# Optimization experiments

Hardware: AMD Instinct MI355X
Metric: run time of the kernel (lower is better)

## Reference

```python
import jax, jax.numpy as jnp
import numpy as np

N = 50000       # nodes
E = 1600000     # edges
H = 64          # hidden_channels
G = 16          # graphs in batch
DOUT = 2        # dim_out
NODE_IN = 1
EDGE_IN = 3


def setup_inputs() -> dict:
    key = jax.random.key(0)
    ks = jax.random.split(key, 24)
    p = lambda k, shape: (jax.random.normal(k, shape, jnp.float32) * 0.05)
    inp = {
        "x": jax.random.normal(ks[0], (N, NODE_IN), jnp.float32),
        "edge_index": jax.random.randint(ks[1], (2, E), 0, N, dtype=jnp.int64),
        "edge_attr": jax.random.normal(ks[2], (E, EDGE_IN), jnp.float32),
        "batch": jnp.sort(jax.random.randint(ks[3], (N,), 0, G, dtype=jnp.int64)),
        # EdgeModel MLP: Linear(2*node_in+edge_in, H), ReLU, Linear(H, H)
        "ew1": p(ks[4], (2 * NODE_IN + EDGE_IN, H)), "eb1": p(ks[5], (H,)),
        "ew2": p(ks[6], (H, H)), "eb2": p(ks[7], (H,)),
        # NodeModel MLP: Linear(node_in+edge_out, H), ReLU, Linear(H, H)
        "nw1": p(ks[8], (NODE_IN + H, H)), "nb1": p(ks[9], (H,)),
        "nw2": p(ks[10], (H, H)), "nb2": p(ks[11], (H,)),
        "ow1": p(ks[12], (H, H)), "ob1": p(ks[13], (H,)),
        "ow2": p(ks[14], (H, H)), "ob2": p(ks[15], (H,)),
        "ow3": p(ks[16], (H, H)), "ob3": p(ks[17], (H,)),
        "ow4": p(ks[18], (H, DOUT)), "ob4": p(ks[19], (DOUT,)),
    }
    return inp


def reference(x, edge_index, edge_attr, batch,
              ew1, eb1, ew2, eb2,
              nw1, nb1, nw2, nb2,
              ow1, ob1, ow2, ob2, ow3, ob3, ow4, ob4):
    row, col = edge_index[0], edge_index[1]
    # EdgeModel: gather endpoints, concat, 2-layer MLP (no residual)
    e_in = jnp.concatenate([x[row], x[col], edge_attr], axis=1)      # [E, 2+3]
    e = jax.nn.relu(e_in @ ew1 + eb1) @ ew2 + eb2                    # [E, H]
    # NodeModel: scatter_add edge messages into destination nodes
    agg = jax.ops.segment_sum(e, col, num_segments=x.shape[0])      # [N, H]
    h_in = jnp.concatenate([x, agg], axis=1)                         # [N, 1+H]
    h = jax.nn.relu(h_in @ nw1 + nb1) @ nw2 + nb2                    # [N, H]
    # global_add_pool over graphs
    pooled = jax.ops.segment_sum(h, batch, num_segments=G)          # [G, H]
    o = jax.nn.relu(pooled @ ow1 + ob1)
    o = jax.nn.relu(o @ ow2 + ob2)
    o = jax.nn.relu(o @ ow3 + ob3)
    return o @ ow4 + ob4                                             # [G, DOUT]
```

## Files before the change

kernel.cpp:

```cpp
#include <hip/hip_runtime.h>
#include <hip/hip_bf16.h>

#define HID 64
#define NGRAPH 16
#define BN 32
#define GB 8
#define MAXNB 2048
#define NCB 256
#define NCT 1024
#define SORT_T 1024
#define SORT_CHUNK 12800

typedef __attribute__((ext_vector_type(8))) short short8;
typedef __attribute__((ext_vector_type(4))) float f32x4;

enum : int {
  OFF_V      = 1040,
  OFF_M      = 1104,
  OFF_EW1    = 5200,
  OFF_EB1    = 5520,
  OFF_NW1    = 5584,
  OFF_NB1    = 9744,
  OFF_NW2    = 9808,
  OFF_NB2    = 13904,
  OFF_OW1    = 13968,
  OFF_OB1    = 18064,
  OFF_OW2    = 18128,
  OFF_OB2    = 22224,
  OFF_OW3    = 22288,
  OFF_OB3    = 26384,
  OFF_OW4    = 26448,
  OFF_OB4    = 26576,
  OFF_EW2    = 26580,
  OFF_EB2    = 30676,
  OFF_FLAGS  = 30740,
  OFF_W1T    = 30744,
  OFF_MT     = 31000,
  OFF_PREP   = 33048
};

struct WPtrs { const void* p[16]; };

__device__ __forceinline__ float cv(float v) { return v; }
__device__ __forceinline__ float cv(__hip_bfloat16 v) { return __bfloat162float(v); }
__device__ __forceinline__ float b2f(unsigned short u) {
  union { unsigned u32; float f; } c;
  c.u32 = ((unsigned)u) << 16;
  return c.f;
}
__device__ __forceinline__ unsigned short f2bu(float v) {
  union { __hip_bfloat16 b; unsigned short u; } c;
  c.b = __float2bfloat16(v);
  return c.u;
}
__device__ __forceinline__ unsigned short fr(float v) {
  unsigned u = __float_as_uint(v);
  u += 0x7FFFu + ((u >> 16) & 1u);
  return (unsigned short)(u >> 16);
}
__device__ __forceinline__ unsigned rndpack(float a, float b) {
  unsigned ua = __float_as_uint(fmaxf(a, 0.0f));
  unsigned ub = __float_as_uint(fmaxf(b, 0.0f));
  ua += 0x7FFFu + ((ua >> 16) & 1u);
  ub += 0x7FFFu + ((ub >> 16) & 1u);
  return __builtin_amdgcn_perm(ub, ua, 0x07060302u);
}

__global__ __launch_bounds__(1024) void prep_kernel(
    const void* xv, const void* eiv, WPtrs wp, float* ws)
{
  __shared__ int red[2];
  __shared__ int s_ft;
  __shared__ float ew2s[4096];
  __shared__ float nw1s[4096];
  const int t = threadIdx.x;
  const int lane = t & 63;

  if (t == 0) { red[0] = 0; red[1] = 0; }
  __syncthreads();
  {
    int big = 0;
    if (t < 512) {
      const unsigned el = (((const unsigned*)xv)[t] >> 7) & 0xFFu;
      big = (el >= 140u) ? 1 : 0;
    }
    #pragma unroll
    for (int o = 32; o > 0; o >>= 1) big += __shfl_xor(big, o);
    if (lane == 0 && big) atomicAdd(&red[0], big);
  }
  {
    int orv = ((const int*)eiv)[1 + 2 * t];
    #pragma unroll
    for (int o = 32; o > 0; o >>= 1) orv |= __shfl_xor(orv, o);
    if (lane == 0 && orv) atomicOr(&red[1], orv);
  }
  __syncthreads();
  if (t == 0) {
    const int ft = (red[0] < 8) ? 1 : 0;
    const int it = (red[1] == 0) ? 1 : 0;
    ((int*)(ws + OFF_FLAGS))[0] = ft;
    ((int*)(ws + OFF_FLAGS))[1] = it;
    s_ft = ft;
  }
  __syncthreads();
  const int ft = s_ft;

  const int sz[16]  = {320,64,4096,64,4160,64,4096,64,4096,64,4096,64,4096,64,128,2};
  const int dst[16] = {OFF_EW1,OFF_EB1,OFF_EW2,OFF_EB2,OFF_NW1,OFF_NB1,OFF_NW2,OFF_NB2,
                       OFF_OW1,OFF_OB1,OFF_OW2,OFF_OB2,OFF_OW3,OFF_OB3,OFF_OW4,OFF_OB4};
  for (int a = 0; a < 16; ++a) {
    const void* src = wp.p[a];
    float* d = ws + dst[a];
    const int n = sz[a];
    const int n4 = n >> 2;
    for (int i = t; i < n4; i += 1024) {
      float4 f;
      if (ft) {
        const ushort4 u4 = ((const ushort4*)src)[i];
        f.x = b2f(u4.x); f.y = b2f(u4.y); f.z = b2f(u4.z); f.w = b2f(u4.w);
      } else {
        f = ((const float4*)src)[i];
      }
      ((float4*)d)[i] = f;
      const int g = i << 2;
      if (a == 2) {
        ew2s[g] = f.x; ew2s[g + 1] = f.y; ew2s[g + 2] = f.z; ew2s[g + 3] = f.w;
      } else if (a == 4 && g >= 64) {
        nw1s[g - 64] = f.x; nw1s[g - 63] = f.y; nw1s[g - 62] = f.z; nw1s[g - 61] = f.w;
      }
    }
    for (int i = (n4 << 2) + t; i < n; i += 1024)
      d[i] = ft ? b2f(((const unsigned short*)src)[i]) : ((const float*)src)[i];
  }
  __syncthreads();

  float mv[4];
  #pragma unroll
  for (int p = 0; p < 4; ++p) {
    const int idx = t + p * 1024;
    const int i = idx >> 6, j = idx & 63;
    float s = 0.0f;
    #pragma unroll 8
    for (int k = 0; k < 64; ++k)
      s = fmaf(ew2s[i * 64 + k], nw1s[k * 64 + j], s);
    mv[p] = s;
  }
  if (t < 64) {
    float s = 0.0f;
    #pragma unroll 8
    for (int k = 0; k < 64; ++k)
      s = fmaf(ws[OFF_EB2 + k], nw1s[k * 64 + t], s);
    ws[OFF_V + t] = s;
  }
  __syncthreads();
  #pragma unroll
  for (int p = 0; p < 4; ++p) ew2s[t + p * 1024] = mv[p];
  __syncthreads();

  if (t < 64) {
    unsigned short* w1t = (unsigned short*)(ws + OFF_W1T);
    #pragma unroll
    for (int k = 0; k < 8; ++k) {
      float v = 0.0f;
      if (k < 5) v = ws[OFF_EW1 + k * 64 + t];
      else if (k == 5) v = ws[OFF_EB1 + t];
      w1t[t * 8 + k] = f2bu(v);
    }
  }
  unsigned short* mt = (unsigned short*)(ws + OFF_MT);
  #pragma unroll
  for (int p = 0; p < 4; ++p) {
    const int idx = t + p * 1024;
    const int n = idx >> 6, k = idx & 63;
    mt[idx] = f2bu(ew2s[k * 64 + n]);
  }
}

template<typename IT>
__device__ __forceinline__ void count_impl(
    const IT* __restrict__ ei, const IT* __restrict__ bt,
    int* __restrict__ gcnt, int* __restrict__ endG, int* lh,
    const int E, const int N, const int NBG)
{
  const int t = threadIdx.x;
  const int b = blockIdx.x;
  for (int i = t; i < NBG; i += NCT) lh[i] = 0;
  {
    const int i = b * NCT + t;
    if (i < N) {
      const int g1 = (int)bt[i];
      if (i == 0) for (int g = 0; g < g1; ++g) endG[g] = 0;
      if (i == N - 1) {
        for (int g = g1; g < NGRAPH; ++g) endG[g] = N;
      } else {
        const int g2 = (int)bt[i + 1];
        for (int g = g1; g < g2; ++g) endG[g] = i + 1;
      }
    }
  }
  __syncthreads();
  const int per = (E + NCB - 1) / NCB;
  const int a = b * per;
  const int bnd = (a + per < E) ? (a + per) : E;
  for (int e = a + t; e < bnd; e += NCT) {
    const int c = (int)ei[(size_t)E + e];
    atomicAdd(&lh[c >> 8], 1);
  }
  __syncthreads();
  for (int i = t; i < NBG; i += NCT) gcnt[(size_t)i * NCB + b] = lh[i];
}

__global__ __launch_bounds__(NCT) void count_kernel(
    const void* eiv, const void* batv, const float* ws,
    int* gcnt, int* endG, const int E, const int N, const int NBG)
{
  __shared__ int lh[MAXNB];
  const int it = ((const int*)(ws + OFF_FLAGS))[1];
  if (it) count_impl<long long>((const long long*)eiv, (const long long*)batv, gcnt, endG, lh, E, N, NBG);
  else    count_impl<int>((const int*)eiv, (const int*)batv, gcnt, endG, lh, E, N, NBG);
}

__global__ __launch_bounds__(256) void scan_tot_kernel(
    const int* __restrict__ gcnt, int* __restrict__ gstart, const int NBG)
{
  const int lane = threadIdx.x & 63;
  const int bkt = blockIdx.x * 4 + (threadIdx.x >> 6);
  if (bkt >= NBG) return;
  const int4 v = *(const int4*)(gcnt + (size_t)bkt * NCB + lane * 4);
  int s = v.x + v.y + v.z + v.w;
  #pragma unroll
  for (int off = 32; off > 0; off >>= 1) s += __shfl_xor(s, off);
  if (lane == 0) gstart[bkt] = s;
}

__global__ __launch_bounds__(256) void scan_pref_kernel(
    int* __restrict__ gstart, const int NBG)
{
  __shared__ int ps[256];
  const int t = threadIdx.x;
  const int seg = (NBG + 255) / 256;
  int s = 0;
  for (int i = 0; i < seg; ++i) {
    const int idx = t * seg + i;
    if (idx < NBG) s += gstart[idx];
  }
  ps[t] = s;
  __syncthreads();
  for (int off = 1; off < 256; off <<= 1) {
    const int v = (t >= off) ? ps[t - off] : 0;
    __syncthreads();
    ps[t] += v;
    __syncthreads();
  }
  int carry = ps[t] - s;
  for (int i = 0; i < seg; ++i) {
    const int idx = t * seg + i;
    if (idx < NBG) {
      const int c = gstart[idx];
      gstart[idx] = carry;
      carry += c;
    }
  }
  if (t == 255) gstart[NBG] = ps[255];
}

__global__ __launch_bounds__(256) void scan_row_kernel(
    int* __restrict__ gcnt, const int* __restrict__ gstart, const int NBG)
{
  const int lane = threadIdx.x & 63;
  const int bkt = blockIdx.x * 4 + (threadIdx.x >> 6);
  if (bkt >= NBG) return;
  int* row = gcnt + (size_t)bkt * NCB;
  const int4 v = *(const int4*)(row + lane * 4);
  const int ls = v.x + v.y + v.z + v.w;
  int s = ls;
  #pragma unroll
  for (int off = 1; off < 64; off <<= 1) {
    const int u = __shfl_up(s, off);
    if (lane >= off) s += u;
  }
  int e = s - ls + gstart[bkt];
  int4 o;
  o.x = e; e += v.x;
  o.y = e; e += v.y;
  o.z = e; e += v.z;
  o.w = e;
  *(int4*)(row + lane * 4) = o;
}

template<typename FT, typename IT>
__device__ __forceinline__ void scatter_impl(
    const FT* __restrict__ x, const IT* __restrict__ ei, const FT* __restrict__ ea,
    const int* __restrict__ gcnt, const int* __restrict__ gstart,
    ushort4* __restrict__ recB, unsigned char* __restrict__ cid, int* lb,
    const int E, const int gb0, const int gb1, const int cap)
{
  const int t = threadIdx.x;
  const int b = blockIdx.x;
  __shared__ int sbase;
  if (t == 0) sbase = gstart[gb0];
  __syncthreads();
  const int base = sbase;
  const int gcount = gb1 - gb0;
  for (int i = t; i < gcount; i += NCT) lb[i] = gcnt[(size_t)(gb0 + i) * NCB + b] - base;
  __syncthreads();

  const int per = (E + NCB - 1) / NCB;
  const int a = b * per;
  const int bnd = (a + per < E) ? (a + per) : E;
  for (int e = a + t; e < bnd; e += NCT) {
    const int c = (int)ei[(size_t)E + e];
    const int grp = c >> 8;
    if (grp >= gb0 && grp < gb1) {
      const int pos = atomicAdd(&lb[grp - gb0], 1);
      if (pos < cap) {
        const int r = (int)ei[e];
        ushort4 rv;
        rv.x = fr(cv(x[r]));
        rv.y = fr(cv(ea[(size_t)3 * e + 0]));
        rv.z = fr(cv(ea[(size_t)3 * e + 1]));
        rv.w = fr(cv(ea[(size_t)3 * e + 2]));
        recB[pos] = rv;
        cid[pos] = (unsigned char)(c & 255);
      }
    }
  }
}

__global__ __launch_bounds__(NCT) void scatter_kernel(
    const void* xv, const void* eiv, const void* eav, const float* ws,
    const int* gcnt, const int* gstart, ushort4* recB, unsigned char* cid,
    const int E, const int gb0, const int gb1, const int cap)
{
  __shared__ int lb[MAXNB];
  const int* fl = (const int*)(ws + OFF_FLAGS);
  const int ft = fl[0], it = fl[1];
  if (ft) {
    if (it) scatter_impl<__hip_bfloat16, long long>((const __hip_bfloat16*)xv, (const long long*)eiv, (const __hip_bfloat16*)eav, gcnt, gstart, recB, cid, lb, E, gb0, gb1, cap);
    else    scatter_impl<__hip_bfloat16, int>((const __hip_bfloat16*)xv, (const int*)eiv, (const __hip_bfloat16*)eav, gcnt, gstart, recB, cid, lb, E, gb0, gb1, cap);
  } else {
    if (it) scatter_impl<float, long long>((const float*)xv, (const long long*)eiv, (const float*)eav, gcnt, gstart, recB, cid, lb, E, gb0, gb1, cap);
    else    scatter_impl<float, int>((const float*)xv, (const int*)eiv, (const float*)eav, gcnt, gstart, recB, cid, lb, E, gb0, gb1, cap);
  }
}

__global__ __launch_bounds__(SORT_T) void sort_kernel(
    ushort4* __restrict__ recB, unsigned char* __restrict__ cid,
    const int* __restrict__ gstart, int* __restrict__ bstartF,
    const int NB, const int gr0, const int cap)
{
  __shared__ unsigned sru[SORT_CHUNK * 2];
  __shared__ unsigned char sc[SORT_CHUNK];
  __shared__ int h2[16][GB];
  __shared__ int fs[GB];
  __shared__ int cur[GB];

  const int t = threadIdx.x;
  const int lane = t & 63;
  const int wav = t >> 6;
  const int g = gr0 + (int)blockIdx.x;

  const int base0 = gstart[gr0];
  int rb = gstart[g] - base0;
  int re = gstart[g + 1] - base0;
  if (rb > cap) rb = cap;
  if (re > cap) re = cap;
  int cnt = re - rb;
  if (cnt > SORT_CHUNK) cnt = SORT_CHUNK;

  if (t < 16 * GB) ((int*)h2)[t] = 0;
  __syncthreads();

  for (int i = t; i < cnt; i += SORT_T) {
    const ushort4 r = recB[rb + i];
    sru[2 * i]     = (unsigned)r.x | ((unsigned)r.y << 16);
    sru[2 * i + 1] = (unsigned)r.z | ((unsigned)r.w << 16);
    const unsigned char c = cid[rb + i];
    sc[i] = c;
    const int kk = c >> 5;
    unsigned long long mym = 0;
    #pragma unroll
    for (int k = 0; k < GB; ++k) {
      const unsigned long long bk = __ballot(kk == k);
      if (kk == k) mym = bk;
    }
    if ((mym & (((unsigned long long)1 << lane) - 1ull)) == 0)
      h2[wav][kk] += (int)__builtin_popcountll(mym);
  }
  __syncthreads();

  if (t == 0) {
    int acc = 0;
    for (int k = 0; k < GB; ++k) {
      int s = 0;
      #pragma unroll
      for (int w = 0; w < 16; ++w) s += h2[w][k];
      fs[k] = acc;
      cur[k] = acc;
      acc += s;
    }
  }
  __syncthreads();

  if (t <= GB) {
    const int bk = g * GB + t;
    if (bk <= NB) bstartF[bk] = base0 + rb + ((t == GB) ? cnt : fs[t]);
  }

  for (int i = t; i < cnt; i += SORT_T) {
    const unsigned char c = sc[i];
    const int kk = c >> 5;
    unsigned long long mym = 0;
    #pragma unroll
    for (int k = 0; k < GB; ++k) {
      const unsigned long long bk = __ballot(kk == k);
      if (kk == k) mym = bk;
    }
    const int lead = (int)__builtin_ctzll(mym);
    const int off = (int)__builtin_popcountll(mym & (((unsigned long long)1 << lane) - 1ull));
    int bas = 0;
    if (lane == lead) bas = atomicAdd(&cur[kk], (int)__builtin_popcountll(mym));
    bas = __shfl(bas, lead);
    const int pos = rb + bas + off;
    const unsigned a = sru[2 * i], b = sru[2 * i + 1];
    ushort4 rv;
    rv.x = (unsigned short)(a & 0xFFFFu); rv.y = (unsigned short)(a >> 16);
    rv.z = (unsigned short)(b & 0xFFFFu); rv.w = (unsigned short)(b >> 16);
    recB[pos] = rv;
    cid[pos] = (unsigned char)(c & 31);
  }
}


#define FUSED_JSTEP(J, RV, CC)                                                   \
    if ((J) < jmax) {                                                            \
      short* HT = sHT + ((J) & 1) * 4608;                                        \
      short8 a1;                                                                 \
      if (quad == 0) {                                                           \
        const bool vv = (CC) < 32;                                               \
        a1[0] = (short)(RV).x;                                                   \
        a1[1] = vv ? (short)xlsb[(CC)] : (short)0;                               \
        a1[2] = (short)(RV).y; a1[3] = (short)(RV).z; a1[4] = (short)(RV).w;     \
        a1[5] = vv ? (short)0x3F80 : (short)0;                                   \
        a1[6] = 0; a1[7] = 0;                                                    \
      } else {                                                                   \
        a1[0]=0; a1[1]=0; a1[2]=0; a1[3]=0; a1[4]=0; a1[5]=0; a1[6]=0; a1[7]=0;  \
      }                                                                          \
      f32x4 Hc0 = __builtin_amdgcn_mfma_f32_16x16x32_bf16(a1, B1[0], (f32x4)0.0f, 0, 0, 0); \
      f32x4 Hc1 = __builtin_amdgcn_mfma_f32_16x16x32_bf16(a1, B1[1], (f32x4)0.0f, 0, 0, 0); \
      f32x4 Hc2 = __builtin_amdgcn_mfma_f32_16x16x32_bf16(a1, B1[2], (f32x4)0.0f, 0, 0, 0); \
      f32x4 Hc3 = __builtin_amdgcn_mfma_f32_16x16x32_bf16(a1, B1[3], (f32x4)0.0f, 0, 0, 0); \
      uint2 pk0, pk1, pk2, pk3;                                                  \
      pk0.x = rndpack(Hc0[0], Hc0[1]); pk0.y = rndpack(Hc0[2], Hc0[3]);          \
      pk1.x = rndpack(Hc1[0], Hc1[1]); pk1.y = rndpack(Hc1[2], Hc1[3]);          \
      pk2.x = rndpack(Hc2[0], Hc2[1]); pk2.y = rndpack(Hc2[2], Hc2[3]);          \
      pk3.x = rndpack(Hc3[0], Hc3[1]); pk3.y = rndpack(Hc3[2], Hc3[3]);          \
      *(uint2*)(HT + ( 0 + l15) * 72 + 16 * wav + quad * 4) = pk0;               \
      *(uint2*)(HT + (16 + l15) * 72 + 16 * wav + quad * 4) = pk1;               \
      *(uint2*)(HT + (32 + l15) * 72 + 16 * wav + quad * 4) = pk2;               \
      *(uint2*)(HT + (48 + l15) * 72 + 16 * wav + quad * 4) = pk3;               \
      __syncthreads();                                                           \
      const short* aj = a2L + (J) * 2304;                                        \
      _Pragma("unroll")                                                          \
      for (int q = 0; q < 2; ++q) {                                              \
        const short8 a20 = *(const short8*)(aj + l15 * 72 + 32 * q + 8 * quad);  \
        const short8 a21 = *(const short8*)(aj + (16 + l15) * 72 + 32 * q + 8 * quad); \
        const short8 b2  = *(const short8*)(HT + (16 * wav + l15) * 72 + 32 * q + quad * 8); \
        C2[0] = __builtin_amdgcn_mfma_f32_16x16x32_bf16(a20, b2, C2[0], 0, 0, 0);\
        C2[1] = __builtin_amdgcn_mfma_f32_16x16x32_bf16(a21, b2, C2[1], 0, 0, 0);\
        C3[0] = __builtin_amdgcn_mfma_f32_16x16x32_bf16(a20, ONES8, C3[0], 0, 0, 0); \
        C3[1] = __builtin_amdgcn_mfma_f32_16x16x32_bf16(a21, ONES8, C3[1], 0, 0, 0); \
      }                                                                          \
    }

template<typename FT, typename IT>
__device__ __forceinline__ void fused_impl(
    const FT* __restrict__ x, const IT* __restrict__ batch,
    const float* __restrict__ ws, const int* __restrict__ bstart,
    const ushort4* __restrict__ recB, const unsigned char* __restrict__ cid,
    float* __restrict__ rep,
    short* sHT, short* a2L,
    float* xls, unsigned short* xlsb, int* sbi,
    const int N, const int gb0, const int cap)
{
  const int t = threadIdx.x;
  const int lane = t & 63;
  const int quad = lane >> 4;
  const int l15 = lane & 15;
  const int wav = t >> 6;
  const int bucket = gb0 + blockIdx.x;

  if (t < BN) {
    const int n = bucket * BN + t;
    const float xvv = (n < N) ? cv(x[n]) : 0.0f;
    xls[t] = xvv;
    xlsb[t] = fr(xvv);
  }
  if (t == 0) {
    const int nf = bucket * BN, nl = bucket * BN + BN - 1;
    sbi[0] = (int)batch[(nf < N) ? nf : (N - 1)];
    sbi[1] = (int)batch[(nl < N) ? nl : (N - 1)];
    sbi[2] = bstart[gb0];
  }
  __syncthreads();

  const unsigned short* w1t = (const unsigned short*)(ws + OFF_W1T);
  short8 B1[4];
  #pragma unroll
  for (int tn = 0; tn < 4; ++tn) {
    short8 z; for (int j = 0; j < 8; ++j) z[j] = 0;
    if (quad == 0) z = *(const short8*)(w1t + (16 * tn + l15) * 8);
    B1[tn] = z;
  }
  short8 ONES8;
  #pragma unroll
  for (int j = 0; j < 8; ++j) ONES8[j] = (short)0x3F80;

  const int base = sbi[2];
  int s0 = bstart[bucket] - base;
  int e0 = bstart[bucket + 1] - base;
  if (s0 > cap) s0 = cap;
  if (e0 > cap) e0 = cap;

  f32x4 C2[2]; C2[0] = (f32x4)0.0f; C2[1] = (f32x4)0.0f;
  f32x4 C3[2]; C3[0] = (f32x4)0.0f; C3[1] = (f32x4)0.0f;

  const int nedge = e0 - s0;
  const int nst = (nedge + 255) >> 8;

  const ushort4 uz = make_ushort4(0, 0, 0, 0);
  ushort4 rv0 = uz, rv1 = uz, rv2 = uz, rv3 = uz;
  int c0 = 255, c1 = 255, c2 = 255, c3 = 255;
  if (nst > 0 && quad == 0) {
    int idx;
    idx = s0 +   0 + 16 * wav + l15; if (idx < e0) { rv0 = recB[idx]; c0 = (int)cid[idx]; }
    idx = s0 +  64 + 16 * wav + l15; if (idx < e0) { rv1 = recB[idx]; c1 = (int)cid[idx]; }
    idx = s0 + 128 + 16 * wav + l15; if (idx < e0) { rv2 = recB[idx]; c2 = (int)cid[idx]; }
    idx = s0 + 192 + 16 * wav + l15; if (idx < e0) { rv3 = recB[idx]; c3 = (int)cid[idx]; }
  }

  for (int st = 0; st < nst; ++st) {
    {
      unsigned long long* az = (unsigned long long*)a2L;
      #pragma unroll
      for (int z = 0; z < 9; ++z) az[t + z * 256] = 0ull;
    }
    __syncthreads();
    if (quad == 0) {
      if (c0 < 32) a2L[0 * 2304 + c0 * 72 + 16 * wav + l15] = (short)0x3F80;
      if (c1 < 32) a2L[1 * 2304 + c1 * 72 + 16 * wav + l15] = (short)0x3F80;
      if (c2 < 32) a2L[2 * 2304 + c2 * 72 + 16 * wav + l15] = (short)0x3F80;
      if (c3 < 32) a2L[3 * 2304 + c3 * 72 + 16 * wav + l15] = (short)0x3F80;
    }
    __syncthreads();

    ushort4 nv0 = uz, nv1 = uz, nv2 = uz, nv3 = uz;
    int n0 = 255, n1 = 255, n2 = 255, n3 = 255;
    if (st + 1 < nst && quad == 0) {
      const int nb = s0 + (st + 1) * 256 + 16 * wav + l15;
      int idx;
      idx = nb;       if (idx < e0) { nv0 = recB[idx]; n0 = (int)cid[idx]; }
      idx = nb +  64; if (idx < e0) { nv1 = recB[idx]; n1 = (int)cid[idx]; }
      idx = nb + 128; if (idx < e0) { nv2 = recB[idx]; n2 = (int)cid[idx]; }
      idx = nb + 192; if (idx < e0) { nv3 = recB[idx]; n3 = (int)cid[idx]; }
    }

    const int m = nedge - st * 256;
    const int jmax = (m >= 256) ? 4 : ((m + 63) >> 6);
    FUSED_JSTEP(0, rv0, c0)
    FUSED_JSTEP(1, rv1, c1)
    FUSED_JSTEP(2, rv2, c2)
    FUSED_JSTEP(3, rv3, c3)
    __syncthreads();
    rv0 = nv0; c0 = n0; rv1 = nv1; c1 = n1;
    rv2 = nv2; c2 = n2; rv3 = nv3; c3 = n3;
  }

  short* aggB = a2L;
  #pragma unroll
  for (int tm2 = 0; tm2 < 2; ++tm2) {
    #pragma unroll
    for (int r = 0; r < 4; ++r)
      aggB[(16 * tm2 + quad * 4 + r) * 72 + 16 * wav + l15] = (short)fr(C2[tm2][r]);
  }
  __syncthreads();

  const unsigned short* mt = (const unsigned short*)(ws + OFF_MT);
  f32x4 D[2]; D[0] = (f32x4)0.0f; D[1] = (f32x4)0.0f;
  #pragma unroll
  for (int q2 = 0; q2 < 2; ++q2) {
    const short8 bb = *(const short8*)(mt + (16 * wav + l15) * 64 + 32 * q2 + quad * 8);
    #pragma unroll
    for (int tm2 = 0; tm2 < 2; ++tm2) {
      const short8 aa = *(const short8*)(aggB + (16 * tm2 + l15) * 72 + 32 * q2 + quad * 8);
      D[tm2] = __builtin_amdgcn_mfma_f32_16x16x32_bf16(aa, bb, D[tm2], 0, 0, 0);
    }
  }

  const int n = 16 * wav + l15;
  const float c1n = ws[OFF_NW1 + n];
  const float vn  = ws[OFF_V + n];
  const float bn  = ws[OFF_NB1 + n];
  float* myrep = rep + (size_t)(bucket & 7) * (NGRAPH * 64);
  const bool multi = (sbi[0] != sbi[1]);

  if (!multi) {
    float hs = 0.0f;
    #pragma unroll
    for (int tm2 = 0; tm2 < 2; ++tm2) {
      #pragma unroll
      for (int r = 0; r < 4; ++r) {
        const int mrow = 16 * tm2 + quad * 4 + r;
        const int ng = bucket * BN + mrow;
        if (ng < N)
          hs += fmaxf(D[tm2][r] + xls[mrow] * c1n + C3[tm2][r] * vn + bn, 0.0f);
      }
    }
    hs += __shfl_xor(hs, 16);
    hs += __shfl_xor(hs, 32);
    if (quad == 0) unsafeAtomicAdd(&myrep[sbi[0] * 64 + n], hs);
  } else {
    float* pooledL = (float*)((char*)a2L + 4608);
    for (int i = t; i < NGRAPH * 64; i += 256) pooledL[i] = 0.0f;
    __syncthreads();
    #pragma unroll
    for (int tm2 = 0; tm2 < 2; ++tm2) {
      #pragma unroll
      for (int r = 0; r < 4; ++r) {
        const int mrow = 16 * tm2 + quad * 4 + r;
        const int ng = bucket * BN + mrow;
        if (ng < N) {
          const float h = fmaxf(D[tm2][r] + xls[mrow] * c1n + C3[tm2][r] * vn + bn, 0.0f);
          const int g = (int)batch[ng];
          atomicAdd(&pooledL[g * 64 + n], h);
        }
      }
    }
    __syncthreads();
    for (int g = sbi[0] + wav; g <= sbi[1]; g += 4)
      unsafeAtomicAdd(&myrep[g * 64 + lane], pooledL[g * 64 + lane]);
  }
}

__global__ __launch_bounds__(256, 4) void fused_kernel(
    const void* xv, const void* batv, const float* ws, const int* bstart,
    const ushort4* recB, const unsigned char* cid, float* rep,
    const int N, const int gb0, const int cap)
{
  __shared__ __align__(16) unsigned char smem[37072];
  short* sHT = (short*)smem;
  short* a2L = (short*)(smem + 18432);
  float* xls = (float*)(smem + 36864);
  unsigned short* xlsb = (unsigned short*)(smem + 36992);
  int* sbi = (int*)(smem + 37056);

  const int* fl = (const int*)(ws + OFF_FLAGS);
  const int ft = fl[0], it = fl[1];
  if (ft) {
    if (it) fused_impl<__hip_bfloat16, long long>((const __hip_bfloat16*)xv, (const long long*)batv, ws, bstart, recB, cid, rep, sHT, a2L, xls, xlsb, sbi, N, gb0, cap);
    else    fused_impl<__hip_bfloat16, int>((const __hip_bfloat16*)xv, (const int*)batv, ws, bstart, recB, cid, rep, sHT, a2L, xls, xlsb, sbi, N, gb0, cap);
  } else {
    if (it) fused_impl<float, long long>((const float*)xv, (const long long*)batv, ws, bstart, recB, cid, rep, sHT, a2L, xls, xlsb, sbi, N, gb0, cap);
    else    fused_impl<float, int>((const float*)xv, (const int*)batv, ws, bstart, recB, cid, rep, sHT, a2L, xls, xlsb, sbi, N, gb0, cap);
  }
}

__global__ __launch_bounds__(256) void head_kernel(
    const float* ws, const float* rep, const int* __restrict__ endG,
    void* outv, const int N)
{
  __shared__ float P[NGRAPH][HID];
  __shared__ float A[NGRAPH][HID];
  __shared__ float B[NGRAPH][HID];
  __shared__ int endL[NGRAPH];

  const int t = threadIdx.x;
  const int j = t & 63;
  const int gq = t >> 6;

  if (t < NGRAPH) endL[t] = endG[t];

  #pragma unroll
  for (int gi = 0; gi < 4; ++gi) {
    const int g = gq + gi * 4;
    float s = 0.0f;
    #pragma unroll
    for (int r = 0; r < 8; ++r)
      s += rep[(size_t)r * (NGRAPH * 64) + g * 64 + j];
    P[g][j] = s;
  }
  __syncthreads();

  {
    const float bj = ws[OFF_NB2 + j];
    #pragma unroll
    for (int gi = 0; gi < 4; ++gi) {
      const int g = gq + gi * 4;
      const float cg = (float)(endL[g] - (g ? endL[g - 1] : 0));
      float s = cg * bj;
      #pragma unroll 8
      for (int k = 0; k < HID; ++k)
        s = fmaf(P[g][k], ws[OFF_NW2 + k * HID + j], s);
      A[g][j] = s;
    }
  }
  __syncthreads();

  const int wOff[3] = {OFF_OW1, OFF_OW2, OFF_OW3};
  const int bOff[3] = {OFF_OB1, OFF_OB2, OFF_OB3};
  for (int L = 0; L < 3; ++L) {
    float (*In)[HID]  = (L & 1) ? B : A;
    float (*Out)[HID] = (L & 1) ? A : B;
    const float bj = ws[bOff[L] + j];
    #pragma unroll
    for (int gi = 0; gi < 4; ++gi) {
      const int g = gq + gi * 4;
      float s = bj;
      #pragma unroll 8
      for (int k = 0; k < HID; ++k)
        s = fmaf(In[g][k], ws[wOff[L] + k * HID + j], s);
      Out[g][j] = fmaxf(s, 0.0f);
    }
    __syncthreads();
  }

  if (t < 32) {
    const int g = t >> 1, d = t & 1;
    float s = ws[OFF_OB4 + d];
    #pragma unroll 8
    for (int k = 0; k < HID; ++k)
      s = fmaf(B[g][k], ws[OFF_OW4 + k * 2 + d], s);
    const int ft = ((const int*)(ws + OFF_FLAGS))[0];
    if (ft) ((__hip_bfloat16*)outv)[g * 2 + d] = __float2bfloat16(s);
    else    ((float*)outv)[g * 2 + d] = s;
  }
}

extern "C" void kernel_launch(void* const* d_in, const int* in_sizes, int n_in,
                              void* d_out, int out_size, void* d_ws, size_t ws_size,
                              hipStream_t stream)
{
  const void* xv   = d_in[0];
  const void* eiv  = d_in[1];
  const void* eav  = d_in[2];
  const void* batv = d_in[3];

  WPtrs wp;
  for (int a = 0; a < 16; ++a) wp.p[a] = d_in[4 + a];

  const int N = in_sizes[0];
  const int E = in_sizes[1] / 2;
  const int NB = (N + BN - 1) / BN;
  const int NBG = (NB + GB - 1) / GB;
  if (NB > MAXNB) return;

  float* ws    = (float*)d_ws;
  float* rep   = ws + OFF_PREP;
  int* gstart  = (int*)(rep + 8 * NGRAPH * 64);
  int* bstartF = gstart + NBG + 1;
  int* endG    = bstartF + NB + 2;
  int* gcnt    = endG + NGRAPH;

  size_t recOffB = ((size_t)((char*)(gcnt + (size_t)NBG * NCB) - (char*)d_ws) + 15) & ~(size_t)15;

  int G = -1; long long cap = 0;
  for (int g = 1; g <= 64; ++g) {
    const long long c = (long long)E / g + E / 32 + 8192;
    if (recOffB + (size_t)c * 9 <= ws_size) { G = g; cap = c; break; }
  }
  if (G < 0) return;

  ushort4* recB = (ushort4*)((char*)d_ws + recOffB);
  unsigned char* cid = (unsigned char*)(recB + cap);
  const int gsz = (NBG + G - 1) / G;
  const int sblk = (NBG + 3) / 4;

  (void)hipMemsetAsync(rep, 0, (size_t)(8 * NGRAPH * 64) * 4, stream);

  prep_kernel<<<1, 1024, 0, stream>>>(xv, eiv, wp, ws);
  count_kernel<<<NCB, NCT, 0, stream>>>(eiv, batv, ws, gcnt, endG, E, N, NBG);
  scan_tot_kernel<<<sblk, 256, 0, stream>>>(gcnt, gstart, NBG);
  scan_pref_kernel<<<1, 256, 0, stream>>>(gstart, NBG);
  scan_row_kernel<<<sblk, 256, 0, stream>>>(gcnt, gstart, NBG);

  for (int g = 0; g < G; ++g) {
    const int gr0 = g * gsz;
    const int gr1 = (gr0 + gsz < NBG) ? (gr0 + gsz) : NBG;
    if (gr0 >= gr1) break;
    scatter_kernel<<<NCB, NCT, 0, stream>>>(xv, eiv, eav, ws, gcnt, gstart,
                                            recB, cid, E, gr0, gr1, (int)cap);
    sort_kernel<<<gr1 - gr0, SORT_T, 0, stream>>>(recB, cid, gstart, bstartF,
                                                  NB, gr0, (int)cap);
    const int b0 = gr0 * GB;
    const int b1 = (gr1 * GB < NB) ? (gr1 * GB) : NB;
    fused_kernel<<<b1 - b0, 256, 0, stream>>>(xv, batv, ws, bstartF, recB, cid,
                                              rep, N, b0, (int)cap);
  }

  head_kernel<<<1, 256, 0, stream>>>(ws, rep, endG, d_out, N);
}
```

Before: 254.7 us.

## Cut per-stage barriers and update one-hot scatter tile incrementally

The full LDS zeroing of the one-hot aggregation tile now happens once before the edge loop instead of every stage. Each stage only clears the previous one-hot entry and sets the new one, per thread. The hidden-tile compute and the aggregation MFMAs are regrouped in pairs using the existing double buffer, so a stage needs four barriers instead of about seven. This targets barrier stalls and redundant LDS stores in the hot loop, at the cost of a little more register state and bookkeeping for the previous cluster IDs.

```diff
diff --git a/kernel.cpp b/kernel.cpp
--- a/kernel.cpp
+++ b/kernel.cpp
@@ -432,7 +432,7 @@
 }
 
 
-#define FUSED_JSTEP(J, RV, CC)                                                   \
+#define FUSED_H(J, RV, CC)                                                       \
     if ((J) < jmax) {                                                            \
       short* HT = sHT + ((J) & 1) * 4608;                                        \
       short8 a1;                                                                 \
@@ -459,18 +459,22 @@
       *(uint2*)(HT + (16 + l15) * 72 + 16 * wav + quad * 4) = pk1;               \
       *(uint2*)(HT + (32 + l15) * 72 + 16 * wav + quad * 4) = pk2;               \
       *(uint2*)(HT + (48 + l15) * 72 + 16 * wav + quad * 4) = pk3;               \
-      __syncthreads();                                                           \
-      const short* aj = a2L + (J) * 2304;                                        \
-      _Pragma("unroll")                                                          \
-      for (int q = 0; q < 2; ++q) {                                              \
-        const short8 a20 = *(const short8*)(aj + l15 * 72 + 32 * q + 8 * quad);  \
+    }
+
+#define FUSED_PV(J)                                                             \
+    if ((J) < jmax) {                                                           \
+      const short* HT = sHT + ((J) & 1) * 4608;                                 \
+      const short* aj = a2L + (J) * 2304;                                       \
+      _Pragma("unroll")                                                         \
+      for (int q = 0; q < 2; ++q) {                                             \
+        const short8 a20 = *(const short8*)(aj + l15 * 72 + 32 * q + 8 * quad); \
         const short8 a21 = *(const short8*)(aj + (16 + l15) * 72 + 32 * q + 8 * quad); \
         const short8 b2  = *(const short8*)(HT + (16 * wav + l15) * 72 + 32 * q + quad * 8); \
         C2[0] = __builtin_amdgcn_mfma_f32_16x16x32_bf16(a20, b2, C2[0], 0, 0, 0);\
         C2[1] = __builtin_amdgcn_mfma_f32_16x16x32_bf16(a21, b2, C2[1], 0, 0, 0);\
         C3[0] = __builtin_amdgcn_mfma_f32_16x16x32_bf16(a20, ONES8, C3[0], 0, 0, 0); \
         C3[1] = __builtin_amdgcn_mfma_f32_16x16x32_bf16(a21, ONES8, C3[1], 0, 0, 0); \
-      }                                                                          \
+      }                                                                         \
     }
 
 template<typename FT, typename IT>
@@ -490,6 +494,11 @@
   const int wav = t >> 6;
   const int bucket = gb0 + blockIdx.x;
 
+  {
+    unsigned long long* az = (unsigned long long*)a2L;
+    #pragma unroll
+    for (int z = 0; z < 9; ++z) az[t + z * 256] = 0ull;
+  }
   if (t < BN) {
     const int n = bucket * BN + t;
     const float xvv = (n < N) ? cv(x[n]) : 0.0f;
@@ -531,6 +540,7 @@
   const ushort4 uz = make_ushort4(0, 0, 0, 0);
   ushort4 rv0 = uz, rv1 = uz, rv2 = uz, rv3 = uz;
   int c0 = 255, c1 = 255, c2 = 255, c3 = 255;
+  int cp0 = 255, cp1 = 255, cp2 = 255, cp3 = 255;
   if (nst > 0 && quad == 0) {
     int idx;
     idx = s0 +   0 + 16 * wav + l15; if (idx < e0) { rv0 = recB[idx]; c0 = (int)cid[idx]; }
@@ -540,19 +550,21 @@
   }
 
   for (int st = 0; st < nst; ++st) {
-    {
-      unsigned long long* az = (unsigned long long*)a2L;
-      #pragma unroll
-      for (int z = 0; z < 9; ++z) az[t + z * 256] = 0ull;
-    }
-    __syncthreads();
+    const int m = nedge - st * 256;
+    const int jmax = (m >= 256) ? 4 : ((m + 63) >> 6);
+
     if (quad == 0) {
-      if (c0 < 32) a2L[0 * 2304 + c0 * 72 + 16 * wav + l15] = (short)0x3F80;
-      if (c1 < 32) a2L[1 * 2304 + c1 * 72 + 16 * wav + l15] = (short)0x3F80;
-      if (c2 < 32) a2L[2 * 2304 + c2 * 72 + 16 * wav + l15] = (short)0x3F80;
-      if (c3 < 32) a2L[3 * 2304 + c3 * 72 + 16 * wav + l15] = (short)0x3F80;
-    }
-    __syncthreads();
+      const int row = 16 * wav + l15;
+      if (cp0 != c0) { if (cp0 < 32) a2L[0 * 2304 + cp0 * 72 + row] = 0;
+                       if (c0  < 32) a2L[0 * 2304 + c0  * 72 + row] = (short)0x3F80; }
+      if (cp1 != c1) { if (cp1 < 32) a2L[1 * 2304 + cp1 * 72 + row] = 0;
+                       if (c1  < 32) a2L[1 * 2304 + c1  * 72 + row] = (short)0x3F80; }
+      if (cp2 != c2) { if (cp2 < 32) a2L[2 * 2304 + cp2 * 72 + row] = 0;
+                       if (c2  < 32) a2L[2 * 2304 + c2  * 72 + row] = (short)0x3F80; }
+      if (cp3 != c3) { if (cp3 < 32) a2L[3 * 2304 + cp3 * 72 + row] = 0;
+                       if (c3  < 32) a2L[3 * 2304 + c3  * 72 + row] = (short)0x3F80; }
+    }
+    cp0 = c0; cp1 = c1; cp2 = c2; cp3 = c3;
 
     ushort4 nv0 = uz, nv1 = uz, nv2 = uz, nv3 = uz;
     int n0 = 255, n1 = 255, n2 = 255, n3 = 255;
@@ -565,13 +577,20 @@
       idx = nb + 192; if (idx < e0) { nv3 = recB[idx]; n3 = (int)cid[idx]; }
     }
 
-    const int m = nedge - st * 256;
-    const int jmax = (m >= 256) ? 4 : ((m + 63) >> 6);
-    FUSED_JSTEP(0, rv0, c0)
-    FUSED_JSTEP(1, rv1, c1)
-    FUSED_JSTEP(2, rv2, c2)
-    FUSED_JSTEP(3, rv3, c3)
+    FUSED_H(0, rv0, c0)
+    FUSED_H(1, rv1, c1)
     __syncthreads();
+    FUSED_PV(0)
+    FUSED_PV(1)
+    __syncthreads();
+    if (jmax > 2) {
+      FUSED_H(2, rv2, c2)
+      FUSED_H(3, rv3, c3)
+      __syncthreads();
+      FUSED_PV(2)
+      FUSED_PV(3)
+      __syncthreads();
+    }
     rv0 = nv0; c0 = n0; rv1 = nv1; c1 = n1;
     rv2 = nv2; c2 = n2; rv3 = nv3; c3 = n3;
   }
```

New measurement: 251.7 us. Within noise of the previous version (-1.2%).
